# Kernel optimization log

Measured on AMD Instinct MI355X. Metric: run time of the kernel, lower is better.

The kernel has to match this reference:

```python
import jax, jax.numpy as jnp
import numpy as np

N_NODES = 20000
N_EDGES = 160000
N_GRAPHS = 16
NEG_INF = -1e30


def gcn_conv(x, edge_index, edge_weight, W, b):
    # PyG GCNConv with improved=True: add self-loops with weight 2.0,
    # symmetric degree normalization, linear transform, scatter-add aggregation.
    N = x.shape[0]
    row, col = edge_index[0], edge_index[1]
    loop = jnp.arange(N)
    row = jnp.concatenate([row, loop])
    col = jnp.concatenate([col, loop])
    ew = jnp.concatenate([edge_weight, jnp.full((N,), 2.0, edge_weight.dtype)])
    deg = jax.ops.segment_sum(ew, col, num_segments=N)
    dinv = jnp.where(deg > 0, deg ** -0.5, 0.0)  # deg_inv_sqrt, inf -> 0
    norm = dinv[row] * ew * dinv[col]            # [E+N]
    xl = x @ W                                   # [N, out]
    out = jax.ops.segment_sum(xl[row] * norm[:, None], col, num_segments=N)
    return out + b


def segment_softmax_masked(logits, mask, batch, num_segments):
    # softmax over masked entries, grouped by graph id (torch_geometric softmax
    # after masked_select); unmasked-out positions return 0.
    neg = jnp.asarray(NEG_INF, logits.dtype)
    ml = jnp.where(mask, logits, neg)
    mx = jax.ops.segment_max(ml, batch, num_segments=num_segments)
    ex = jnp.where(mask, jnp.exp(logits - mx[batch]), 0.0)
    s = jax.ops.segment_sum(ex, batch, num_segments=num_segments)
    return ex / jnp.maximum(s[batch], 1e-16)


def setup_inputs() -> dict:
    key = jax.random.key(0)
    ks = jax.random.split(key, 12)
    x = jax.random.normal(ks[0], (N_NODES, 5), dtype=jnp.float32)
    edge_index = jax.random.randint(ks[1], (2, N_EDGES), 0, N_NODES)
    edge_weight = jax.random.uniform(ks[2], (N_EDGES,), dtype=jnp.float32)
    mask = jax.random.randint(ks[3], (N_NODES,), 0, 2).astype(bool)
    batch = jnp.sort(jax.random.randint(ks[4], (N_NODES,), 0, N_GRAPHS))
    # parameters (Glorot-ish scaling)
    W1 = jax.random.normal(ks[5], (5, 1000), dtype=jnp.float32) / np.sqrt(5)
    b1 = jnp.zeros((1000,), jnp.float32)
    W2 = jax.random.normal(ks[6], (1000, 1000), dtype=jnp.float32) / np.sqrt(1000)
    b2 = jnp.zeros((1000,), jnp.float32)
    Wf = jax.random.normal(ks[7], (1000, 1), dtype=jnp.float32) / np.sqrt(1000)
    bf = jnp.zeros((1,), jnp.float32)
    return {"x": x, "edge_weight": edge_weight, "W1": W1, "b1": b1,
            "W2": W2, "b2": b2, "Wf": Wf, "bf": bf,
            "edge_index": edge_index, "mask": mask, "batch": batch}


def reference(x, edge_weight, W1, b1, W2, b2, Wf, bf, edge_index, mask, batch):
    h = jax.nn.relu(gcn_conv(x, edge_index, edge_weight, W1, b1))
    h = jax.nn.relu(gcn_conv(h, edge_index, edge_weight, W2, b2))
    # dropout treated as identity (eval mode) for a deterministic reference
    logits = (h @ Wf + bf)[:, 0]  # [N]
    return segment_softmax_masked(logits, mask, batch, N_GRAPHS)
```

## Files before the change

### kernel.cpp

```cpp
#include <hip/hip_runtime.h>

#define NN 20000
#define NE 160000
#define NG 16
#define KP 1024
#define MT2 160
#define MPAD2 (MT2*128)
#define NBLK 79

typedef __attribute__((ext_vector_type(8))) short bf16x8;
typedef __attribute__((ext_vector_type(4))) float f32x4;

#define GAS __attribute__((address_space(1)))
#define LAS __attribute__((address_space(3)))

__device__ __forceinline__ unsigned short f2bf(float f) {
    unsigned int u = __float_as_uint(f);
    u += 0x7FFFu + ((u >> 16) & 1u);
    return (unsigned short)(u >> 16);
}

__device__ __forceinline__ void gld_lds16(const char* g, char* l) {
    __builtin_amdgcn_global_load_lds((GAS void*)g, (LAS void*)l, 16, 0, 0);
}

__global__ void deg_cnt_kernel(const int* __restrict__ ei, const float* __restrict__ ew,
                               float* deg, int* cnt, const void* __restrict__ mask,
                               int* flags) {
    const int e = blockIdx.x * blockDim.x + threadIdx.x;
    if (e < 5000) {
        const unsigned v = ((const unsigned*)mask)[e];
        if (v > 1u) atomicOr(&flags[0], 1);
        if (v != 0u && v != 0x3F800000u) atomicOr(&flags[1], 1);
    }
    if (e >= NE) return;
    const int c = ei[NE + e];
    atomicAdd(&deg[c], ew[e]);
    atomicAdd(&cnt[c], 1);
}

__global__ __launch_bounds__(256) void partial_w2t_kernel(const int* __restrict__ cnt,
        const float* __restrict__ deg, const void* __restrict__ mask,
        const int* __restrict__ flags, int* __restrict__ mtmp,
        float* __restrict__ dinv, int* __restrict__ bcnt, int* __restrict__ bmsk,
        const float* __restrict__ W2, unsigned short* __restrict__ W2t,
        float* __restrict__ logitsC) {
    const int bid = blockIdx.x;
    const int t = threadIdx.x;
    if (bid < NBLK) {
        const int i = bid * 256 + t;
        const int f0 = flags[0], f1 = flags[1];
        int c = 0, mv = 0;
        if (i < NN) {
            c = cnt[i];
            dinv[i] = 1.0f / sqrtf(2.0f + deg[i]);
            if (f0 == 0)      mv = ((const int*)mask)[i] != 0;
            else if (f1 == 0) mv = ((const unsigned*)mask)[i] != 0u;
            else              mv = ((const unsigned char*)mask)[i] != 0;
            mtmp[i] = mv;
        }
        __shared__ int sc[256], sm[256];
        sc[t] = c; sm[t] = mv;
        __syncthreads();
        for (int off = 128; off; off >>= 1) {
            if (t < off) { sc[t] += sc[t + off]; sm[t] += sm[t + off]; }
            __syncthreads();
        }
        if (t == 0) { bcnt[bid] = sc[0]; bmsk[bid] = sm[0]; }
    } else {
        __shared__ float tile[32][33];
        const int bw = bid - NBLK;
        if (t < 20) logitsC[bw * 20 + t] = 0.0f;
        const int n0 = (bw & 31) * 32;
        const int k0 = (bw >> 5) * 32;
        const int tx = t & 31, ty = t >> 5;
#pragma unroll
        for (int j = 0; j < 4; ++j) {
            const int k = k0 + ty + j * 8;
            const int n = n0 + tx;
            tile[ty + j * 8][tx] = (k < 1000 && n < 1000) ? W2[k * 1000 + n] : 0.0f;
        }
        __syncthreads();
#pragma unroll
        for (int j = 0; j < 4; ++j) {
            const int n = n0 + ty + j * 8;
            const int k = k0 + tx;
            W2t[(size_t)n * KP + k] = f2bf(tile[tx][ty + j * 8]);
        }
    }
}

__global__ __launch_bounds__(256) void apply_kernel(const int* __restrict__ cnt,
        const int* __restrict__ mtmp, const int* __restrict__ bcnt,
        const int* __restrict__ bmsk, const int* __restrict__ batch,
        int* __restrict__ offs, int* __restrict__ perm, int* __restrict__ bc,
        int* __restrict__ nm, int* __restrict__ cursor, float* __restrict__ out) {
    const int b = blockIdx.x, t = threadIdx.x;
    __shared__ int pbc[128], pbm[128];
    if (t < 128) {
        pbc[t] = (t < NBLK) ? bcnt[t] : 0;
        pbm[t] = (t < NBLK) ? bmsk[t] : 0;
    }
    __syncthreads();
    for (int off = 1; off < 128; off <<= 1) {
        int uc = 0, um = 0;
        if (t < 128 && t >= off) { uc = pbc[t - off]; um = pbm[t - off]; }
        __syncthreads();
        if (t < 128) { pbc[t] += uc; pbm[t] += um; }
        __syncthreads();
    }
    if (b == 0 && t == 0) nm[0] = pbm[NBLK - 1];
    const int bco = (b == 0) ? 0 : pbc[b - 1];
    const int bmo = (b == 0) ? 0 : pbm[b - 1];
    const int i = b * 256 + t;
    const int c  = (i < NN) ? cnt[i]  : 0;
    const int mv = (i < NN) ? mtmp[i] : 0;
    __shared__ int sc[256], sm[256];
    sc[t] = c; sm[t] = mv;
    __syncthreads();
    for (int off = 1; off < 256; off <<= 1) {
        const int uc = (t >= off) ? sc[t - off] : 0;
        const int um = (t >= off) ? sm[t - off] : 0;
        __syncthreads();
        sc[t] += uc; sm[t] += um;
        __syncthreads();
    }
    if (i < NN) {
        cursor[i] = 0;
        out[i] = 0.0f;
        offs[i] = bco + sc[t] - c;
        if (mv) {
            const int pos = bmo + sm[t] - 1;
            perm[pos] = i;
            bc[pos] = batch[i];
        }
    }
}

__global__ void scatter_kernel(const int* __restrict__ ei, const float* __restrict__ ew,
                               const float* __restrict__ dinv, const int* __restrict__ offs,
                               int* cursor, int* __restrict__ ssrc, float* __restrict__ snorm) {
    const int e = blockIdx.x * blockDim.x + threadIdx.x;
    if (e >= NE) return;
    const int r = ei[e], c = ei[NE + e];
    const int pos = atomicAdd(&cursor[c], 1);
    const int idx = offs[c] + pos;
    ssrc[idx] = r;
    snorm[idx] = dinv[r] * ew[e] * dinv[c];
}

__global__ __launch_bounds__(256) void axf_kernel(const float* __restrict__ x,
        const int* __restrict__ ssrc, const float* __restrict__ snorm,
        const int* __restrict__ offs, const int* __restrict__ cnt,
        const float* __restrict__ dinv, float* __restrict__ Axf) {
    const int i = blockIdx.x * blockDim.x + threadIdx.x;
    if (i >= NN) return;
    float a0=0,a1=0,a2=0,a3=0,a4=0;
    const int s0 = offs[i], n = cnt[i];
    for (int e = s0; e < s0 + n; ++e) {
        const int r = ssrc[e];
        const float w = snorm[e];
        const float* xr = x + r * 5;
        a0 += w*xr[0]; a1 += w*xr[1]; a2 += w*xr[2]; a3 += w*xr[3]; a4 += w*xr[4];
    }
    const float wl = 2.0f * dinv[i] * dinv[i];
    const float* xi = x + i * 5;
    a0 += wl*xi[0]; a1 += wl*xi[1]; a2 += wl*xi[2]; a3 += wl*xi[3]; a4 += wl*xi[4];
    float* o = Axf + i * 5;
    o[0]=a0; o[1]=a1; o[2]=a2; o[3]=a3; o[4]=a4;
}

__global__ __launch_bounds__(256) void aggW1_kernel(const float* __restrict__ Axf,
        const float* __restrict__ W1, const float* __restrict__ b1,
        const int* __restrict__ ssrc, const float* __restrict__ snorm,
        const int* __restrict__ offs, const int* __restrict__ cnt,
        const float* __restrict__ dinv, const int* __restrict__ perm,
        const int* __restrict__ nm, unsigned short* __restrict__ G) {
    const int tid = threadIdx.x;
    const int wv = tid >> 6;
    const int lane = tid & 63;
    const int half = wv & 1;
    const int jbase = blockIdx.x * 8 + (wv >> 1) * 4;
    const int nmv = nm[0];
    const int npad = (nmv + 127) & ~127;
    if (jbase >= npad) return;

    const int c0 = half * 512 + lane * 8;
    float w1r[5][8], bbr[8];
#pragma unroll
    for (int q = 0; q < 2; ++q) {
        const int c = c0 + q * 4;
        const bool v = (c <= 996);
#pragma unroll
        for (int f = 0; f < 5; ++f) {
            const float4 w4 = v ? *(const float4*)(W1 + f * 1000 + c)
                                : make_float4(0.f, 0.f, 0.f, 0.f);
            w1r[f][q*4+0] = w4.x; w1r[f][q*4+1] = w4.y;
            w1r[f][q*4+2] = w4.z; w1r[f][q*4+3] = w4.w;
        }
        const float4 b4 = v ? *(const float4*)(b1 + c) : make_float4(0.f, 0.f, 0.f, 0.f);
        bbr[q*4+0] = b4.x; bbr[q*4+1] = b4.y; bbr[q*4+2] = b4.z; bbr[q*4+3] = b4.w;
    }

    int iv[4], s0a[4], na[4]; float dva[4];
#pragma unroll
    for (int d = 0; d < 4; ++d) {
        const int j = jbase + d;
        iv[d] = (j < nmv) ? perm[j] : -1;
    }
#pragma unroll
    for (int d = 0; d < 4; ++d) {
        if (iv[d] >= 0) { s0a[d] = offs[iv[d]]; na[d] = cnt[iv[d]]; dva[d] = dinv[iv[d]]; }
        else            { s0a[d] = 0; na[d] = -1; dva[d] = 0.f; }
    }

#pragma unroll
    for (int d = 0; d < 4; ++d) {
        const int j = jbase + d;
        float acc[8];
#pragma unroll
        for (int k = 0; k < 8; ++k) acc[k] = 0.f;
        const int i = iv[d];
        if (i >= 0) {
            const int s0 = s0a[d], n = na[d];
            const int total = n + 1;
            for (int base = 0; base < total; base += 64) {
                const int m = (total - base < 64) ? (total - base) : 64;
                float a0=0.f, a1=0.f, a2=0.f, a3=0.f, a4=0.f, we=0.f;
                if (lane < m) {
                    const int idx = base + lane;
                    int r;
                    if (idx < n) { r = ssrc[s0 + idx]; we = snorm[s0 + idx]; }
                    else         { r = i; we = 2.0f * dva[d] * dva[d]; }
                    const float* axr = Axf + r * 5;
                    a0 = axr[0]; a1 = axr[1]; a2 = axr[2]; a3 = axr[3]; a4 = axr[4];
                }
#pragma unroll 2
                for (int e = 0; e < m; ++e) {
                    const float s0v = __shfl(a0, e);
                    const float s1v = __shfl(a1, e);
                    const float s2v = __shfl(a2, e);
                    const float s3v = __shfl(a3, e);
                    const float s4v = __shfl(a4, e);
                    const float swv = __shfl(we, e);
#pragma unroll
                    for (int k = 0; k < 8; ++k) {
                        const float z = bbr[k] + s0v * w1r[0][k] + s1v * w1r[1][k]
                                      + s2v * w1r[2][k] + s3v * w1r[3][k] + s4v * w1r[4][k];
                        acc[k] += swv * fmaxf(z, 0.f);
                    }
                }
            }
        }
        bf16x8 pk;
#pragma unroll
        for (int k = 0; k < 8; ++k) pk[k] = (short)f2bf(acc[k]);
        *(bf16x8*)(G + (size_t)j * KP + c0) = pk;
    }
}

__global__ __launch_bounds__(256) void gemm_kernel(const unsigned short* __restrict__ A,
                                                   const unsigned short* __restrict__ B,
                                                   const float* __restrict__ b2,
                                                   const float* __restrict__ Wf,
                                                   const int* __restrict__ nm,
                                                   float* __restrict__ logitsC) {
    __shared__ unsigned short As[4096];
    __shared__ unsigned short Bs[4096];
    const int tid = threadIdx.x;
    __shared__ int s_nm;
    if (tid == 0) s_nm = nm[0];
    __syncthreads();
    const int nmv = s_nm;
    const int mstrips = (nmv + 127) >> 7;
    const int bid = blockIdx.x;
    const int tm = (bid >> 6) * 8 + (bid & 7);
    const int tn = (bid >> 3) & 7;
    if (tm >= mstrips) return;
    const int lane = tid & 63;
    const int wv = tid >> 6;
    const int wr = wv >> 1, wc = wv & 1;

    const int chunk = ((tid & 3) ^ ((tid >> 3) & 3)) * 16;
    const int rsub = tid >> 2;
    const char* Ag = (const char*)(A + (size_t)(tm * 128 + rsub) * KP) + chunk;
    const char* Bg = (const char*)(B + (size_t)(tn * 128 + rsub) * KP) + chunk;
    char* AsW = (char*)As + wv * 1024;
    char* BsW = (char*)Bs + wv * 1024;

    f32x4 acc[4][4];
#pragma unroll
    for (int i = 0; i < 4; ++i)
#pragma unroll
        for (int j = 0; j < 4; ++j) acc[i][j] = (f32x4){0.f, 0.f, 0.f, 0.f};

    const int m = lane & 15;
    const int quad = lane >> 4;
    const int sw = quad ^ ((m >> 1) & 3);
    const int aoff = (wr * 64 + m) * 64 + sw * 16;
    const int boff = (wc * 64 + m) * 64 + sw * 16;

    for (int kk = 0; kk < KP; kk += 32) {
        __syncthreads();
        const int kb = kk * 2;
        gld_lds16(Ag + kb,             AsW);
        gld_lds16(Ag + kb + 64 * 2048, AsW + 4096);
        gld_lds16(Bg + kb,             BsW);
        gld_lds16(Bg + kb + 64 * 2048, BsW + 4096);
        __syncthreads();
        bf16x8 af[4], bfv[4];
#pragma unroll
        for (int mt = 0; mt < 4; ++mt)
            af[mt] = *(const bf16x8*)((const char*)As + aoff + mt * 1024);
#pragma unroll
        for (int nt = 0; nt < 4; ++nt)
            bfv[nt] = *(const bf16x8*)((const char*)Bs + boff + nt * 1024);
#pragma unroll
        for (int mt = 0; mt < 4; ++mt)
#pragma unroll
            for (int nt = 0; nt < 4; ++nt)
                acc[mt][nt] = __builtin_amdgcn_mfma_f32_16x16x32_bf16(af[mt], bfv[nt], acc[mt][nt], 0, 0, 0);
    }

    const int col0 = tn * 128 + wc * 64 + m;
    const int row00 = tm * 128 + wr * 64 + quad * 4;
#pragma unroll
    for (int mt = 0; mt < 4; ++mt) {
        float ps0 = 0.f, ps1 = 0.f, ps2 = 0.f, ps3 = 0.f;
#pragma unroll
        for (int nt = 0; nt < 4; ++nt) {
            const int c = col0 + nt * 16;
            const float bbv = (c < 1000) ? b2[c] : 0.0f;
            const float wfv = (c < 1000) ? Wf[c] : 0.0f;
            ps0 += fmaxf(acc[mt][nt][0] + bbv, 0.f) * wfv;
            ps1 += fmaxf(acc[mt][nt][1] + bbv, 0.f) * wfv;
            ps2 += fmaxf(acc[mt][nt][2] + bbv, 0.f) * wfv;
            ps3 += fmaxf(acc[mt][nt][3] + bbv, 0.f) * wfv;
        }
#pragma unroll
        for (int msk = 1; msk < 16; msk <<= 1) {
            ps0 += __shfl_xor(ps0, msk);
            ps1 += __shfl_xor(ps1, msk);
            ps2 += __shfl_xor(ps2, msk);
            ps3 += __shfl_xor(ps3, msk);
        }
        if (m == 0) {
            const int row = row00 + mt * 16;
            if (row + 0 < nmv) atomicAdd(&logitsC[row + 0], ps0);
            if (row + 1 < nmv) atomicAdd(&logitsC[row + 1], ps1);
            if (row + 2 < nmv) atomicAdd(&logitsC[row + 2], ps2);
            if (row + 3 < nmv) atomicAdd(&logitsC[row + 3], ps3);
        }
    }
}

__global__ __launch_bounds__(256) void softmax_kernel(const float* __restrict__ logitsC,
        const int* __restrict__ perm, const int* __restrict__ bc,
        const int* __restrict__ nm, float* __restrict__ out) {
    const int g = blockIdx.x;
    const int t = threadIdx.x;
    __shared__ int s_lo, s_hi;
    __shared__ float red[4];
    __shared__ float sval;
    if (t == 0) {
        const int nmv = nm[0];
        int lo = 0, hi = nmv;
        while (lo < hi) { const int mid = (lo + hi) >> 1; if (bc[mid] < g) lo = mid + 1; else hi = mid; }
        s_lo = lo;
        int lo2 = lo, hi2 = nmv;
        while (lo2 < hi2) { const int mid = (lo2 + hi2) >> 1; if (bc[mid] < g + 1) lo2 = mid + 1; else hi2 = mid; }
        s_hi = lo2;
    }
    __syncthreads();
    const int lo = s_lo, hi = s_hi;
    float mx = -1e30f;
    for (int i = lo + t; i < hi; i += 256) mx = fmaxf(mx, logitsC[i]);
    for (int off = 32; off; off >>= 1) mx = fmaxf(mx, __shfl_down(mx, off));
    if ((t & 63) == 0) red[t >> 6] = mx;
    __syncthreads();
    if (t == 0) sval = fmaxf(fmaxf(red[0], red[1]), fmaxf(red[2], red[3]));
    __syncthreads();
    mx = sval;
    __syncthreads();
    float sm = 0.f;
    for (int i = lo + t; i < hi; i += 256) sm += expf(logitsC[i] - mx);
    for (int off = 32; off; off >>= 1) sm += __shfl_down(sm, off);
    if ((t & 63) == 0) red[t >> 6] = sm;
    __syncthreads();
    if (t == 0) sval = red[0] + red[1] + red[2] + red[3];
    __syncthreads();
    const float inv = 1.0f / fmaxf(sval, 1e-16f);
    for (int i = lo + t; i < hi; i += 256)
        out[perm[i]] = expf(logitsC[i] - mx) * inv;
}

extern "C" void kernel_launch(void* const* d_in, const int* in_sizes, int n_in,
                              void* d_out, int out_size, void* d_ws, size_t ws_size,
                              hipStream_t stream) {
    (void)in_sizes; (void)n_in; (void)out_size; (void)ws_size;
    const float* x   = (const float*)d_in[0];
    const float* ew  = (const float*)d_in[1];
    const float* W1  = (const float*)d_in[2];
    const float* b1  = (const float*)d_in[3];
    const float* W2  = (const float*)d_in[4];
    const float* b2  = (const float*)d_in[5];
    const float* Wf  = (const float*)d_in[6];
    const int*   ei  = (const int*)d_in[8];
    const void*  mask  = d_in[9];
    const int*   batch = (const int*)d_in[10];
    float* out = (float*)d_out;

    char* p = (char*)d_ws;
    auto carve = [&](size_t bytes) { char* q = p; p += (bytes + 255) & ~(size_t)255; return q; };
    char* zbase = p;
    float* deg     = (float*)carve(NN * 4);
    int*   cnt     = (int*)carve(NN * 4);
    int*   flags   = (int*)carve(256);
    size_t zspan = (size_t)(p - zbase);
    int*   cursor  = (int*)carve(NN * 4);
    float* logitsC = (float*)carve(MPAD2 * 4);
    int*   offs   = (int*)carve(NN * 4);
    float* dinv   = (float*)carve(NN * 4);
    int*   mtmp   = (int*)carve(NN * 4);
    int*   perm   = (int*)carve(NN * 4);
    int*   bc     = (int*)carve(NN * 4);
    int*   bcnt   = (int*)carve(NBLK * 4);
    int*   bmsk   = (int*)carve(NBLK * 4);
    int*   nmp    = (int*)carve(256);
    int*   ssrc   = (int*)carve(NE * 4);
    float* snorm  = (float*)carve(NE * 4);
    float* Axf    = (float*)carve(NN * 5 * 4);
    unsigned short* W2t = (unsigned short*)carve((size_t)KP * KP * 2);
    unsigned short* G   = (unsigned short*)carve((size_t)MPAD2 * KP * 2);

    hipMemsetAsync(zbase, 0, zspan, stream);
    hipLaunchKernelGGL(deg_cnt_kernel,     dim3(625),       dim3(256), 0, stream, ei, ew, deg, cnt, mask, flags);
    hipLaunchKernelGGL(partial_w2t_kernel, dim3(NBLK+1024), dim3(256), 0, stream, cnt, deg, mask, flags, mtmp, dinv, bcnt, bmsk, W2, W2t, logitsC);
    hipLaunchKernelGGL(apply_kernel,       dim3(NBLK),      dim3(256), 0, stream, cnt, mtmp, bcnt, bmsk, batch, offs, perm, bc, nmp, cursor, out);
    hipLaunchKernelGGL(scatter_kernel,     dim3(625),       dim3(256), 0, stream, ei, ew, dinv, offs, cursor, ssrc, snorm);
    hipLaunchKernelGGL(axf_kernel,         dim3(79),        dim3(256), 0, stream, x, ssrc, snorm, offs, cnt, dinv, Axf);
    hipLaunchKernelGGL(aggW1_kernel,       dim3(MPAD2/8),   dim3(256), 0, stream, Axf, W1, b1, ssrc, snorm, offs, cnt, dinv, perm, nmp, G);
    hipLaunchKernelGGL(gemm_kernel,        dim3(MT2*8),     dim3(256), 0, stream, G, W2t, b2, Wf, nmp, logitsC);
    hipLaunchKernelGGL(softmax_kernel,     dim3(NG),        dim3(256), 0, stream, logitsC, perm, bc, nmp, out);
}
```

Before: 198.5 us.

## Fuse preprocessing stages into one cooperative kernel with grid syncs

Merges the memset and five preprocessing kernels (degree count, partial sums plus W2 transpose, scan/apply, CSR scatter, first-layer aggregation) into a single cooperative kernel of 640 blocks, separated by grid-wide barriers. The W2 transpose now runs concurrently with the degree atomics on a disjoint set of blocks. The aim is to cut kernel launch and inter-kernel gaps. In exchange, each phase runs on a fixed grid with grid.sync costs, some phases use only 79 blocks, and cooperative launch has extra overhead.

```diff
diff --git a/kernel.cpp b/kernel.cpp
--- a/kernel.cpp
+++ b/kernel.cpp
@@ -1,4 +1,7 @@
 #include <hip/hip_runtime.h>
+#include <hip/hip_cooperative_groups.h>
+
+namespace cg = cooperative_groups;
 
 #define NN 20000
 #define NE 160000
@@ -7,6 +10,7 @@
 #define MT2 160
 #define MPAD2 (MT2*128)
 #define NBLK 79
+#define PREP_GRID 640
 
 typedef __attribute__((ext_vector_type(8))) short bf16x8;
 typedef __attribute__((ext_vector_type(4))) float f32x4;
@@ -24,31 +28,71 @@
     __builtin_amdgcn_global_load_lds((GAS void*)g, (LAS void*)l, 16, 0, 0);
 }
 
-__global__ void deg_cnt_kernel(const int* __restrict__ ei, const float* __restrict__ ew,
-                               float* deg, int* cnt, const void* __restrict__ mask,
-                               int* flags) {
-    const int e = blockIdx.x * blockDim.x + threadIdx.x;
-    if (e < 5000) {
-        const unsigned v = ((const unsigned*)mask)[e];
-        if (v > 1u) atomicOr(&flags[0], 1);
-        if (v != 0u && v != 0x3F800000u) atomicOr(&flags[1], 1);
-    }
-    if (e >= NE) return;
-    const int c = ei[NE + e];
-    atomicAdd(&deg[c], ew[e]);
-    atomicAdd(&cnt[c], 1);
-}
-
-__global__ __launch_bounds__(256) void partial_w2t_kernel(const int* __restrict__ cnt,
-        const float* __restrict__ deg, const void* __restrict__ mask,
-        const int* __restrict__ flags, int* __restrict__ mtmp,
-        float* __restrict__ dinv, int* __restrict__ bcnt, int* __restrict__ bmsk,
-        const float* __restrict__ W2, unsigned short* __restrict__ W2t,
+__global__ __launch_bounds__(256) void prep_kernel(
+        const int* __restrict__ ei, const float* __restrict__ ew,
+        const float* __restrict__ x, const float* __restrict__ W2,
+        const int* __restrict__ batch, const void* __restrict__ mask,
+        float* __restrict__ deg, int* __restrict__ cnt, int* __restrict__ flags,
+        int* __restrict__ mtmp, float* __restrict__ dinv,
+        int* __restrict__ bcnt, int* __restrict__ bmsk,
+        int* __restrict__ offs, int* __restrict__ perm, int* __restrict__ bc,
+        int* __restrict__ nm, int* __restrict__ cursor, float* __restrict__ out,
+        int* __restrict__ ssrc, float* __restrict__ snorm,
+        float* __restrict__ Axf, unsigned short* __restrict__ W2t,
         float* __restrict__ logitsC) {
+    cg::grid_group grid = cg::this_grid();
     const int bid = blockIdx.x;
     const int t = threadIdx.x;
-    if (bid < NBLK) {
-        const int i = bid * 256 + t;
+    const int nb = gridDim.x;
+    const int gt = bid * 256 + t;
+    const int gn = nb * 256;
+
+    __shared__ union ShU {
+        float tile[32][33];
+        struct { int sc[256]; int sm[256]; int pbc[128]; int pbm[128]; } s;
+    } sh;
+
+    for (int i = gt; i < NN; i += gn) { deg[i] = 0.0f; cnt[i] = 0; }
+    if (gt < 8) flags[gt] = 0;
+    grid.sync();
+
+    if (bid < 128) {
+        for (int vb = bid; vb < 1024; vb += 128) {
+            if (t < 20) logitsC[vb * 20 + t] = 0.0f;
+            const int n0 = (vb & 31) * 32;
+            const int k0 = (vb >> 5) * 32;
+            const int tx = t & 31, ty = t >> 5;
+            __syncthreads();
+#pragma unroll
+            for (int j = 0; j < 4; ++j) {
+                const int k = k0 + ty + j * 8;
+                const int n = n0 + tx;
+                sh.tile[ty + j * 8][tx] = (k < 1000 && n < 1000) ? W2[k * 1000 + n] : 0.0f;
+            }
+            __syncthreads();
+#pragma unroll
+            for (int j = 0; j < 4; ++j) {
+                const int n = n0 + ty + j * 8;
+                const int k = k0 + tx;
+                W2t[(size_t)n * KP + k] = f2bf(sh.tile[tx][ty + j * 8]);
+            }
+        }
+    } else {
+        for (int e = (bid - 128) * 256 + t; e < NE; e += (PREP_GRID - 128) * 256) {
+            if (e < 5000) {
+                const unsigned v = ((const unsigned*)mask)[e];
+                if (v > 1u) atomicOr(&flags[0], 1);
+                if (v != 0u && v != 0x3F800000u) atomicOr(&flags[1], 1);
+            }
+            const int c = ei[NE + e];
+            atomicAdd(&deg[c], ew[e]);
+            atomicAdd(&cnt[c], 1);
+        }
+    }
+    grid.sync();
+
+    for (int vb = bid; vb < NBLK; vb += nb) {
+        const int i = vb * 256 + t;
         const int f0 = flags[0], f1 = flags[1];
         int c = 0, mv = 0;
         if (i < NN) {
@@ -59,115 +103,83 @@
             else              mv = ((const unsigned char*)mask)[i] != 0;
             mtmp[i] = mv;
         }
-        __shared__ int sc[256], sm[256];
-        sc[t] = c; sm[t] = mv;
+        sh.s.sc[t] = c; sh.s.sm[t] = mv;
         __syncthreads();
         for (int off = 128; off; off >>= 1) {
-            if (t < off) { sc[t] += sc[t + off]; sm[t] += sm[t + off]; }
-            __syncthreads();
-        }
-        if (t == 0) { bcnt[bid] = sc[0]; bmsk[bid] = sm[0]; }
-    } else {
-        __shared__ float tile[32][33];
-        const int bw = bid - NBLK;
-        if (t < 20) logitsC[bw * 20 + t] = 0.0f;
-        const int n0 = (bw & 31) * 32;
-        const int k0 = (bw >> 5) * 32;
-        const int tx = t & 31, ty = t >> 5;
-#pragma unroll
-        for (int j = 0; j < 4; ++j) {
-            const int k = k0 + ty + j * 8;
-            const int n = n0 + tx;
-            tile[ty + j * 8][tx] = (k < 1000 && n < 1000) ? W2[k * 1000 + n] : 0.0f;
-        }
-        __syncthreads();
-#pragma unroll
-        for (int j = 0; j < 4; ++j) {
-            const int n = n0 + ty + j * 8;
-            const int k = k0 + tx;
-            W2t[(size_t)n * KP + k] = f2bf(tile[tx][ty + j * 8]);
-        }
-    }
-}
-
-__global__ __launch_bounds__(256) void apply_kernel(const int* __restrict__ cnt,
-        const int* __restrict__ mtmp, const int* __restrict__ bcnt,
-        const int* __restrict__ bmsk, const int* __restrict__ batch,
-        int* __restrict__ offs, int* __restrict__ perm, int* __restrict__ bc,
-        int* __restrict__ nm, int* __restrict__ cursor, float* __restrict__ out) {
-    const int b = blockIdx.x, t = threadIdx.x;
-    __shared__ int pbc[128], pbm[128];
-    if (t < 128) {
-        pbc[t] = (t < NBLK) ? bcnt[t] : 0;
-        pbm[t] = (t < NBLK) ? bmsk[t] : 0;
-    }
-    __syncthreads();
-    for (int off = 1; off < 128; off <<= 1) {
-        int uc = 0, um = 0;
-        if (t < 128 && t >= off) { uc = pbc[t - off]; um = pbm[t - off]; }
-        __syncthreads();
-        if (t < 128) { pbc[t] += uc; pbm[t] += um; }
-        __syncthreads();
-    }
-    if (b == 0 && t == 0) nm[0] = pbm[NBLK - 1];
-    const int bco = (b == 0) ? 0 : pbc[b - 1];
-    const int bmo = (b == 0) ? 0 : pbm[b - 1];
-    const int i = b * 256 + t;
-    const int c  = (i < NN) ? cnt[i]  : 0;
-    const int mv = (i < NN) ? mtmp[i] : 0;
-    __shared__ int sc[256], sm[256];
-    sc[t] = c; sm[t] = mv;
-    __syncthreads();
-    for (int off = 1; off < 256; off <<= 1) {
-        const int uc = (t >= off) ? sc[t - off] : 0;
-        const int um = (t >= off) ? sm[t - off] : 0;
-        __syncthreads();
-        sc[t] += uc; sm[t] += um;
-        __syncthreads();
-    }
-    if (i < NN) {
-        cursor[i] = 0;
-        out[i] = 0.0f;
-        offs[i] = bco + sc[t] - c;
-        if (mv) {
-            const int pos = bmo + sm[t] - 1;
-            perm[pos] = i;
-            bc[pos] = batch[i];
-        }
-    }
-}
-
-__global__ void scatter_kernel(const int* __restrict__ ei, const float* __restrict__ ew,
-                               const float* __restrict__ dinv, const int* __restrict__ offs,
-                               int* cursor, int* __restrict__ ssrc, float* __restrict__ snorm) {
-    const int e = blockIdx.x * blockDim.x + threadIdx.x;
-    if (e >= NE) return;
-    const int r = ei[e], c = ei[NE + e];
-    const int pos = atomicAdd(&cursor[c], 1);
-    const int idx = offs[c] + pos;
-    ssrc[idx] = r;
-    snorm[idx] = dinv[r] * ew[e] * dinv[c];
-}
-
-__global__ __launch_bounds__(256) void axf_kernel(const float* __restrict__ x,
-        const int* __restrict__ ssrc, const float* __restrict__ snorm,
-        const int* __restrict__ offs, const int* __restrict__ cnt,
-        const float* __restrict__ dinv, float* __restrict__ Axf) {
-    const int i = blockIdx.x * blockDim.x + threadIdx.x;
-    if (i >= NN) return;
-    float a0=0,a1=0,a2=0,a3=0,a4=0;
-    const int s0 = offs[i], n = cnt[i];
-    for (int e = s0; e < s0 + n; ++e) {
-        const int r = ssrc[e];
-        const float w = snorm[e];
-        const float* xr = x + r * 5;
-        a0 += w*xr[0]; a1 += w*xr[1]; a2 += w*xr[2]; a3 += w*xr[3]; a4 += w*xr[4];
-    }
-    const float wl = 2.0f * dinv[i] * dinv[i];
-    const float* xi = x + i * 5;
-    a0 += wl*xi[0]; a1 += wl*xi[1]; a2 += wl*xi[2]; a3 += wl*xi[3]; a4 += wl*xi[4];
-    float* o = Axf + i * 5;
-    o[0]=a0; o[1]=a1; o[2]=a2; o[3]=a3; o[4]=a4;
+            if (t < off) { sh.s.sc[t] += sh.s.sc[t + off]; sh.s.sm[t] += sh.s.sm[t + off]; }
+            __syncthreads();
+        }
+        if (t == 0) { bcnt[vb] = sh.s.sc[0]; bmsk[vb] = sh.s.sm[0]; }
+        __syncthreads();
+    }
+    grid.sync();
+
+    for (int vb = bid; vb < NBLK; vb += nb) {
+        if (t < 128) {
+            sh.s.pbc[t] = (t < NBLK) ? bcnt[t] : 0;
+            sh.s.pbm[t] = (t < NBLK) ? bmsk[t] : 0;
+        }
+        __syncthreads();
+        for (int off = 1; off < 128; off <<= 1) {
+            int uc = 0, um = 0;
+            if (t < 128 && t >= off) { uc = sh.s.pbc[t - off]; um = sh.s.pbm[t - off]; }
+            __syncthreads();
+            if (t < 128) { sh.s.pbc[t] += uc; sh.s.pbm[t] += um; }
+            __syncthreads();
+        }
+        if (vb == 0 && t == 0) nm[0] = sh.s.pbm[NBLK - 1];
+        const int bco = (vb == 0) ? 0 : sh.s.pbc[vb - 1];
+        const int bmo = (vb == 0) ? 0 : sh.s.pbm[vb - 1];
+        const int i = vb * 256 + t;
+        const int c  = (i < NN) ? cnt[i]  : 0;
+        const int mv = (i < NN) ? mtmp[i] : 0;
+        sh.s.sc[t] = c; sh.s.sm[t] = mv;
+        __syncthreads();
+        for (int off = 1; off < 256; off <<= 1) {
+            const int uc = (t >= off) ? sh.s.sc[t - off] : 0;
+            const int um = (t >= off) ? sh.s.sm[t - off] : 0;
+            __syncthreads();
+            sh.s.sc[t] += uc; sh.s.sm[t] += um;
+            __syncthreads();
+        }
+        if (i < NN) {
+            cursor[i] = 0;
+            out[i] = 0.0f;
+            offs[i] = bco + sh.s.sc[t] - c;
+            if (mv) {
+                const int pos = bmo + sh.s.sm[t] - 1;
+                perm[pos] = i;
+                bc[pos] = batch[i];
+            }
+        }
+        __syncthreads();
+    }
+    grid.sync();
+
+    for (int e = gt; e < NE; e += gn) {
+        const int r = ei[e], c = ei[NE + e];
+        const int pos = atomicAdd(&cursor[c], 1);
+        const int idx = offs[c] + pos;
+        ssrc[idx] = r;
+        snorm[idx] = dinv[r] * ew[e] * dinv[c];
+    }
+    grid.sync();
+
+    for (int i = gt; i < NN; i += gn) {
+        float a0 = 0, a1 = 0, a2 = 0, a3 = 0, a4 = 0;
+        const int s0 = offs[i], n = cnt[i];
+        for (int e = s0; e < s0 + n; ++e) {
+            const int r = ssrc[e];
+            const float w = snorm[e];
+            const float* xr = x + r * 5;
+            a0 += w * xr[0]; a1 += w * xr[1]; a2 += w * xr[2]; a3 += w * xr[3]; a4 += w * xr[4];
+        }
+        const float wl = 2.0f * dinv[i] * dinv[i];
+        const float* xi = x + i * 5;
+        a0 += wl * xi[0]; a1 += wl * xi[1]; a2 += wl * xi[2]; a3 += wl * xi[3]; a4 += wl * xi[4];
+        float* o = Axf + i * 5;
+        o[0] = a0; o[1] = a1; o[2] = a2; o[3] = a3; o[4] = a4;
+    }
 }
 
 __global__ __launch_bounds__(256) void aggW1_kernel(const float* __restrict__ Axf,
@@ -412,11 +424,9 @@
 
     char* p = (char*)d_ws;
     auto carve = [&](size_t bytes) { char* q = p; p += (bytes + 255) & ~(size_t)255; return q; };
-    char* zbase = p;
     float* deg     = (float*)carve(NN * 4);
     int*   cnt     = (int*)carve(NN * 4);
     int*   flags   = (int*)carve(256);
-    size_t zspan = (size_t)(p - zbase);
     int*   cursor  = (int*)carve(NN * 4);
     float* logitsC = (float*)carve(MPAD2 * 4);
     int*   offs   = (int*)carve(NN * 4);
@@ -433,13 +443,19 @@
     unsigned short* W2t = (unsigned short*)carve((size_t)KP * KP * 2);
     unsigned short* G   = (unsigned short*)carve((size_t)MPAD2 * KP * 2);
 
-    hipMemsetAsync(zbase, 0, zspan, stream);
-    hipLaunchKernelGGL(deg_cnt_kernel,     dim3(625),       dim3(256), 0, stream, ei, ew, deg, cnt, mask, flags);
-    hipLaunchKernelGGL(partial_w2t_kernel, dim3(NBLK+1024), dim3(256), 0, stream, cnt, deg, mask, flags, mtmp, dinv, bcnt, bmsk, W2, W2t, logitsC);
-    hipLaunchKernelGGL(apply_kernel,       dim3(NBLK),      dim3(256), 0, stream, cnt, mtmp, bcnt, bmsk, batch, offs, perm, bc, nmp, cursor, out);
-    hipLaunchKernelGGL(scatter_kernel,     dim3(625),       dim3(256), 0, stream, ei, ew, dinv, offs, cursor, ssrc, snorm);
-    hipLaunchKernelGGL(axf_kernel,         dim3(79),        dim3(256), 0, stream, x, ssrc, snorm, offs, cnt, dinv, Axf);
-    hipLaunchKernelGGL(aggW1_kernel,       dim3(MPAD2/8),   dim3(256), 0, stream, Axf, W1, b1, ssrc, snorm, offs, cnt, dinv, perm, nmp, G);
-    hipLaunchKernelGGL(gemm_kernel,        dim3(MT2*8),     dim3(256), 0, stream, G, W2t, b2, Wf, nmp, logitsC);
-    hipLaunchKernelGGL(softmax_kernel,     dim3(NG),        dim3(256), 0, stream, logitsC, perm, bc, nmp, out);
-}
+    void* pargs[] = {
+        (void*)&ei, (void*)&ew, (void*)&x, (void*)&W2, (void*)&batch, (void*)&mask,
+        (void*)&deg, (void*)&cnt, (void*)&flags, (void*)&mtmp, (void*)&dinv,
+        (void*)&bcnt, (void*)&bmsk, (void*)&offs, (void*)&perm, (void*)&bc,
+        (void*)&nmp, (void*)&cursor, (void*)&out, (void*)&ssrc, (void*)&snorm,
+        (void*)&Axf, (void*)&W2t, (void*)&logitsC
+    };
+    hipLaunchCooperativeKernel((void*)prep_kernel, dim3(PREP_GRID), dim3(256),
+                               pargs, 0, stream);
+    hipLaunchKernelGGL(aggW1_kernel, dim3(MPAD2/8), dim3(256), 0, stream,
+                       Axf, W1, b1, ssrc, snorm, offs, cnt, dinv, perm, nmp, G);
+    hipLaunchKernelGGL(gemm_kernel,  dim3(MT2*8),   dim3(256), 0, stream,
+                       G, W2t, b2, Wf, nmp, logitsC);
+    hipLaunchKernelGGL(softmax_kernel, dim3(NG),    dim3(256), 0, stream,
+                       logitsC, perm, bc, nmp, out);
+}
```

After: 560.7 us. 2.82x slower.

## Merge scan into single-block mid kernel and fuse Axf into edge scatter

Applied to the files above, without the earlier changes.

Replaces the two-kernel block-partial/apply prefix scan with a single-block serial-per-thread scan inside a combined kernel that also computes dinv, zeroes Axf and transposes W2. The Axf aggregation is folded into the edge scatter kernel using float atomics, removing the separate axf pass. This cuts launch count and kernel boundaries but introduces a one-block scan with strided, uncoalesced reads on the critical path and many float atomics with nondeterministic summation order.

```diff
diff --git a/kernel.cpp b/kernel.cpp
--- a/kernel.cpp
+++ b/kernel.cpp
@@ -39,40 +39,70 @@
     atomicAdd(&cnt[c], 1);
 }
 
-__global__ __launch_bounds__(256) void partial_w2t_kernel(const int* __restrict__ cnt,
-        const float* __restrict__ deg, const void* __restrict__ mask,
-        const int* __restrict__ flags, int* __restrict__ mtmp,
-        float* __restrict__ dinv, int* __restrict__ bcnt, int* __restrict__ bmsk,
-        const float* __restrict__ W2, unsigned short* __restrict__ W2t,
-        float* __restrict__ logitsC) {
+__global__ __launch_bounds__(256) void mid_kernel(
+        const float* __restrict__ deg, const int* __restrict__ cnt,
+        const int* __restrict__ flags, const void* __restrict__ mask,
+        const int* __restrict__ batch, const float* __restrict__ W2,
+        float* __restrict__ dinv, float* __restrict__ Axf,
+        int* __restrict__ offs, int* __restrict__ perm, int* __restrict__ bcv,
+        int* __restrict__ nm, int* __restrict__ cursor, float* __restrict__ out,
+        unsigned short* __restrict__ W2t, float* __restrict__ logitsC) {
     const int bid = blockIdx.x;
     const int t = threadIdx.x;
-    if (bid < NBLK) {
-        const int i = bid * 256 + t;
+    __shared__ float tile[32][33];
+    __shared__ int wtc[4], wtm[4];
+
+    if (bid == 0) {
         const int f0 = flags[0], f1 = flags[1];
-        int c = 0, mv = 0;
+        const bool wordmask = (f0 == 0 || f1 == 0);
+        const int lane = t & 63, wvi = t >> 6;
+        const int i0 = t * 79;
+        int tc = 0, tm = 0;
+        for (int j = 0; j < 79; ++j) {
+            const int i = i0 + j;
+            if (i < NN) {
+                tc += cnt[i];
+                tm += wordmask ? (((const unsigned*)mask)[i] != 0u)
+                               : (((const unsigned char*)mask)[i] != 0);
+            }
+        }
+        const int myc = tc, mym = tm;
+        for (int o = 1; o < 64; o <<= 1) {
+            const int uc = __shfl_up(tc, o);
+            const int um = __shfl_up(tm, o);
+            if (lane >= o) { tc += uc; tm += um; }
+        }
+        if (lane == 63) { wtc[wvi] = tc; wtm[wvi] = tm; }
+        __syncthreads();
+        int bc0 = 0, bm0 = 0;
+        for (int w = 0; w < wvi; ++w) { bc0 += wtc[w]; bm0 += wtm[w]; }
+        int runc = bc0 + tc - myc;
+        int runm = bm0 + tm - mym;
+        if (t == 0) nm[0] = wtm[0] + wtm[1] + wtm[2] + wtm[3];
+        for (int j = 0; j < 79; ++j) {
+            const int i = i0 + j;
+            if (i < NN) {
+                const int c = cnt[i];
+                const int mv = wordmask ? (((const unsigned*)mask)[i] != 0u)
+                                        : (((const unsigned char*)mask)[i] != 0);
+                offs[i] = runc; runc += c;
+                cursor[i] = 0;
+                out[i] = 0.0f;
+                if (mv) { perm[runm] = i; bcv[runm] = batch[i]; ++runm; }
+            }
+        }
+    } else if (bid < 80) {
+        const int i = (bid - 1) * 256 + t;
         if (i < NN) {
-            c = cnt[i];
             dinv[i] = 1.0f / sqrtf(2.0f + deg[i]);
-            if (f0 == 0)      mv = ((const int*)mask)[i] != 0;
-            else if (f1 == 0) mv = ((const unsigned*)mask)[i] != 0u;
-            else              mv = ((const unsigned char*)mask)[i] != 0;
-            mtmp[i] = mv;
-        }
-        __shared__ int sc[256], sm[256];
-        sc[t] = c; sm[t] = mv;
-        __syncthreads();
-        for (int off = 128; off; off >>= 1) {
-            if (t < off) { sc[t] += sc[t + off]; sm[t] += sm[t + off]; }
-            __syncthreads();
-        }
-        if (t == 0) { bcnt[bid] = sc[0]; bmsk[bid] = sm[0]; }
+            float* a = Axf + i * 5;
+            a[0] = 0.f; a[1] = 0.f; a[2] = 0.f; a[3] = 0.f; a[4] = 0.f;
+        }
     } else {
-        __shared__ float tile[32][33];
-        const int bw = bid - NBLK;
-        if (t < 20) logitsC[bw * 20 + t] = 0.0f;
-        const int n0 = (bw & 31) * 32;
-        const int k0 = (bw >> 5) * 32;
+        const int vb = bid - 80;
+        if (t < 20) logitsC[vb * 20 + t] = 0.0f;
+        const int n0 = (vb & 31) * 32;
+        const int k0 = (vb >> 5) * 32;
         const int tx = t & 31, ty = t >> 5;
 #pragma unroll
         for (int j = 0; j < 4; ++j) {
@@ -90,84 +120,37 @@
     }
 }
 
-__global__ __launch_bounds__(256) void apply_kernel(const int* __restrict__ cnt,
-        const int* __restrict__ mtmp, const int* __restrict__ bcnt,
-        const int* __restrict__ bmsk, const int* __restrict__ batch,
-        int* __restrict__ offs, int* __restrict__ perm, int* __restrict__ bc,
-        int* __restrict__ nm, int* __restrict__ cursor, float* __restrict__ out) {
-    const int b = blockIdx.x, t = threadIdx.x;
-    __shared__ int pbc[128], pbm[128];
-    if (t < 128) {
-        pbc[t] = (t < NBLK) ? bcnt[t] : 0;
-        pbm[t] = (t < NBLK) ? bmsk[t] : 0;
-    }
-    __syncthreads();
-    for (int off = 1; off < 128; off <<= 1) {
-        int uc = 0, um = 0;
-        if (t < 128 && t >= off) { uc = pbc[t - off]; um = pbm[t - off]; }
-        __syncthreads();
-        if (t < 128) { pbc[t] += uc; pbm[t] += um; }
-        __syncthreads();
-    }
-    if (b == 0 && t == 0) nm[0] = pbm[NBLK - 1];
-    const int bco = (b == 0) ? 0 : pbc[b - 1];
-    const int bmo = (b == 0) ? 0 : pbm[b - 1];
-    const int i = b * 256 + t;
-    const int c  = (i < NN) ? cnt[i]  : 0;
-    const int mv = (i < NN) ? mtmp[i] : 0;
-    __shared__ int sc[256], sm[256];
-    sc[t] = c; sm[t] = mv;
-    __syncthreads();
-    for (int off = 1; off < 256; off <<= 1) {
-        const int uc = (t >= off) ? sc[t - off] : 0;
-        const int um = (t >= off) ? sm[t - off] : 0;
-        __syncthreads();
-        sc[t] += uc; sm[t] += um;
-        __syncthreads();
-    }
-    if (i < NN) {
-        cursor[i] = 0;
-        out[i] = 0.0f;
-        offs[i] = bco + sc[t] - c;
-        if (mv) {
-            const int pos = bmo + sm[t] - 1;
-            perm[pos] = i;
-            bc[pos] = batch[i];
-        }
-    }
-}
-
-__global__ void scatter_kernel(const int* __restrict__ ei, const float* __restrict__ ew,
-                               const float* __restrict__ dinv, const int* __restrict__ offs,
-                               int* cursor, int* __restrict__ ssrc, float* __restrict__ snorm) {
+__global__ void scatter_axf_kernel(const int* __restrict__ ei, const float* __restrict__ ew,
+                                   const float* __restrict__ x, const float* __restrict__ dinv,
+                                   const int* __restrict__ offs, int* cursor,
+                                   int* __restrict__ ssrc, float* __restrict__ snorm,
+                                   float* __restrict__ Axf) {
     const int e = blockIdx.x * blockDim.x + threadIdx.x;
-    if (e >= NE) return;
-    const int r = ei[e], c = ei[NE + e];
-    const int pos = atomicAdd(&cursor[c], 1);
-    const int idx = offs[c] + pos;
-    ssrc[idx] = r;
-    snorm[idx] = dinv[r] * ew[e] * dinv[c];
-}
-
-__global__ __launch_bounds__(256) void axf_kernel(const float* __restrict__ x,
-        const int* __restrict__ ssrc, const float* __restrict__ snorm,
-        const int* __restrict__ offs, const int* __restrict__ cnt,
-        const float* __restrict__ dinv, float* __restrict__ Axf) {
-    const int i = blockIdx.x * blockDim.x + threadIdx.x;
-    if (i >= NN) return;
-    float a0=0,a1=0,a2=0,a3=0,a4=0;
-    const int s0 = offs[i], n = cnt[i];
-    for (int e = s0; e < s0 + n; ++e) {
-        const int r = ssrc[e];
-        const float w = snorm[e];
+    if (e < NE) {
+        const int r = ei[e], c = ei[NE + e];
+        const int pos = atomicAdd(&cursor[c], 1);
+        const int idx = offs[c] + pos;
+        const float w = dinv[r] * ew[e] * dinv[c];
+        ssrc[idx] = r;
+        snorm[idx] = w;
         const float* xr = x + r * 5;
-        a0 += w*xr[0]; a1 += w*xr[1]; a2 += w*xr[2]; a3 += w*xr[3]; a4 += w*xr[4];
-    }
-    const float wl = 2.0f * dinv[i] * dinv[i];
-    const float* xi = x + i * 5;
-    a0 += wl*xi[0]; a1 += wl*xi[1]; a2 += wl*xi[2]; a3 += wl*xi[3]; a4 += wl*xi[4];
-    float* o = Axf + i * 5;
-    o[0]=a0; o[1]=a1; o[2]=a2; o[3]=a3; o[4]=a4;
+        float* ac = Axf + c * 5;
+        atomicAdd(ac + 0, w * xr[0]);
+        atomicAdd(ac + 1, w * xr[1]);
+        atomicAdd(ac + 2, w * xr[2]);
+        atomicAdd(ac + 3, w * xr[3]);
+        atomicAdd(ac + 4, w * xr[4]);
+    }
+    if (e < NN) {
+        const float wl = 2.0f * dinv[e] * dinv[e];
+        const float* xi = x + e * 5;
+        float* ai = Axf + e * 5;
+        atomicAdd(ai + 0, wl * xi[0]);
+        atomicAdd(ai + 1, wl * xi[1]);
+        atomicAdd(ai + 2, wl * xi[2]);
+        atomicAdd(ai + 3, wl * xi[3]);
+        atomicAdd(ai + 4, wl * xi[4]);
+    }
 }
 
 __global__ __launch_bounds__(256) void aggW1_kernel(const float* __restrict__ Axf,
@@ -421,11 +404,8 @@
     float* logitsC = (float*)carve(MPAD2 * 4);
     int*   offs   = (int*)carve(NN * 4);
     float* dinv   = (float*)carve(NN * 4);
-    int*   mtmp   = (int*)carve(NN * 4);
     int*   perm   = (int*)carve(NN * 4);
     int*   bc     = (int*)carve(NN * 4);
-    int*   bcnt   = (int*)carve(NBLK * 4);
-    int*   bmsk   = (int*)carve(NBLK * 4);
     int*   nmp    = (int*)carve(256);
     int*   ssrc   = (int*)carve(NE * 4);
     float* snorm  = (float*)carve(NE * 4);
@@ -434,12 +414,10 @@
     unsigned short* G   = (unsigned short*)carve((size_t)MPAD2 * KP * 2);
 
     hipMemsetAsync(zbase, 0, zspan, stream);
-    hipLaunchKernelGGL(deg_cnt_kernel,     dim3(625),       dim3(256), 0, stream, ei, ew, deg, cnt, mask, flags);
-    hipLaunchKernelGGL(partial_w2t_kernel, dim3(NBLK+1024), dim3(256), 0, stream, cnt, deg, mask, flags, mtmp, dinv, bcnt, bmsk, W2, W2t, logitsC);
-    hipLaunchKernelGGL(apply_kernel,       dim3(NBLK),      dim3(256), 0, stream, cnt, mtmp, bcnt, bmsk, batch, offs, perm, bc, nmp, cursor, out);
-    hipLaunchKernelGGL(scatter_kernel,     dim3(625),       dim3(256), 0, stream, ei, ew, dinv, offs, cursor, ssrc, snorm);
-    hipLaunchKernelGGL(axf_kernel,         dim3(79),        dim3(256), 0, stream, x, ssrc, snorm, offs, cnt, dinv, Axf);
-    hipLaunchKernelGGL(aggW1_kernel,       dim3(MPAD2/8),   dim3(256), 0, stream, Axf, W1, b1, ssrc, snorm, offs, cnt, dinv, perm, nmp, G);
-    hipLaunchKernelGGL(gemm_kernel,        dim3(MT2*8),     dim3(256), 0, stream, G, W2t, b2, Wf, nmp, logitsC);
-    hipLaunchKernelGGL(softmax_kernel,     dim3(NG),        dim3(256), 0, stream, logitsC, perm, bc, nmp, out);
-}
+    hipLaunchKernelGGL(deg_cnt_kernel,   dim3(625),     dim3(256), 0, stream, ei, ew, deg, cnt, mask, flags);
+    hipLaunchKernelGGL(mid_kernel,       dim3(1104),    dim3(256), 0, stream, deg, cnt, flags, mask, batch, W2, dinv, Axf, offs, perm, bc, nmp, cursor, out, W2t, logitsC);
+    hipLaunchKernelGGL(scatter_axf_kernel, dim3(625),   dim3(256), 0, stream, ei, ew, x, dinv, offs, cursor, ssrc, snorm, Axf);
+    hipLaunchKernelGGL(aggW1_kernel,     dim3(MPAD2/8), dim3(256), 0, stream, Axf, W1, b1, ssrc, snorm, offs, cnt, dinv, perm, nmp, G);
+    hipLaunchKernelGGL(gemm_kernel,      dim3(MT2*8),   dim3(256), 0, stream, G, W2t, b2, Wf, nmp, logitsC);
+    hipLaunchKernelGGL(softmax_kernel,   dim3(NG),      dim3(256), 0, stream, logitsC, perm, bc, nmp, out);
+}
```

Result: slower. 350.6 us (+76.6%).

## Merge degree counting with W2 transpose, redo prefix scan, double GEMM K-step

Applied to the files above, without the earlier changes.

The edge degree/count atomics now run in the same launch as the W2 bf16 transpose, so those independent jobs share one grid. The block-partial reduction kernel is dropped: each apply block re-reduces all preceding counts and mask values itself, and a small kernel computes dinv. The GEMM loads a K-slice of 64 per iteration into doubled LDS tiles, halving the barrier count. The trade-off is redundant prefix work in the apply kernel (up to about 20K reads for the last blocks), more LDS per GEMM block that may lower occupancy, and the same number of launches overall.

```diff
diff --git a/kernel.cpp b/kernel.cpp
--- a/kernel.cpp
+++ b/kernel.cpp
@@ -24,55 +24,30 @@
     __builtin_amdgcn_global_load_lds((GAS void*)g, (LAS void*)l, 16, 0, 0);
 }
 
-__global__ void deg_cnt_kernel(const int* __restrict__ ei, const float* __restrict__ ew,
-                               float* deg, int* cnt, const void* __restrict__ mask,
-                               int* flags) {
-    const int e = blockIdx.x * blockDim.x + threadIdx.x;
-    if (e < 5000) {
-        const unsigned v = ((const unsigned*)mask)[e];
-        if (v > 1u) atomicOr(&flags[0], 1);
-        if (v != 0u && v != 0x3F800000u) atomicOr(&flags[1], 1);
-    }
-    if (e >= NE) return;
-    const int c = ei[NE + e];
-    atomicAdd(&deg[c], ew[e]);
-    atomicAdd(&cnt[c], 1);
-}
-
-__global__ __launch_bounds__(256) void partial_w2t_kernel(const int* __restrict__ cnt,
-        const float* __restrict__ deg, const void* __restrict__ mask,
-        const int* __restrict__ flags, int* __restrict__ mtmp,
-        float* __restrict__ dinv, int* __restrict__ bcnt, int* __restrict__ bmsk,
+__global__ __launch_bounds__(256) void degcnt_w2t_kernel(
+        const int* __restrict__ ei, const float* __restrict__ ew,
+        const void* __restrict__ mask, float* deg, int* cnt, int* flags,
         const float* __restrict__ W2, unsigned short* __restrict__ W2t,
         float* __restrict__ logitsC) {
     const int bid = blockIdx.x;
     const int t = threadIdx.x;
-    if (bid < NBLK) {
-        const int i = bid * 256 + t;
-        const int f0 = flags[0], f1 = flags[1];
-        int c = 0, mv = 0;
-        if (i < NN) {
-            c = cnt[i];
-            dinv[i] = 1.0f / sqrtf(2.0f + deg[i]);
-            if (f0 == 0)      mv = ((const int*)mask)[i] != 0;
-            else if (f1 == 0) mv = ((const unsigned*)mask)[i] != 0u;
-            else              mv = ((const unsigned char*)mask)[i] != 0;
-            mtmp[i] = mv;
-        }
-        __shared__ int sc[256], sm[256];
-        sc[t] = c; sm[t] = mv;
-        __syncthreads();
-        for (int off = 128; off; off >>= 1) {
-            if (t < off) { sc[t] += sc[t + off]; sm[t] += sm[t + off]; }
-            __syncthreads();
-        }
-        if (t == 0) { bcnt[bid] = sc[0]; bmsk[bid] = sm[0]; }
+    __shared__ float tile[32][33];
+    if (bid < 625) {
+        const int e = bid * 256 + t;
+        if (e < 5000) {
+            const unsigned v = ((const unsigned*)mask)[e];
+            if (v > 1u) atomicOr(&flags[0], 1);
+            if (v != 0u && v != 0x3F800000u) atomicOr(&flags[1], 1);
+        }
+        if (e >= NE) return;
+        const int c = ei[NE + e];
+        atomicAdd(&deg[c], ew[e]);
+        atomicAdd(&cnt[c], 1);
     } else {
-        __shared__ float tile[32][33];
-        const int bw = bid - NBLK;
-        if (t < 20) logitsC[bw * 20 + t] = 0.0f;
-        const int n0 = (bw & 31) * 32;
-        const int k0 = (bw >> 5) * 32;
+        const int vb = bid - 625;
+        if (t < 20) logitsC[vb * 20 + t] = 0.0f;
+        const int n0 = (vb & 31) * 32;
+        const int k0 = (vb >> 5) * 32;
         const int tx = t & 31, ty = t >> 5;
 #pragma unroll
         for (int j = 0; j < 4; ++j) {
@@ -91,31 +66,36 @@
 }
 
 __global__ __launch_bounds__(256) void apply_kernel(const int* __restrict__ cnt,
-        const int* __restrict__ mtmp, const int* __restrict__ bcnt,
-        const int* __restrict__ bmsk, const int* __restrict__ batch,
-        int* __restrict__ offs, int* __restrict__ perm, int* __restrict__ bc,
-        int* __restrict__ nm, int* __restrict__ cursor, float* __restrict__ out) {
+        const void* __restrict__ mask, const int* __restrict__ flags,
+        const int* __restrict__ batch, int* __restrict__ offs,
+        int* __restrict__ perm, int* __restrict__ bc, int* __restrict__ nm,
+        int* __restrict__ cursor, float* __restrict__ out) {
     const int b = blockIdx.x, t = threadIdx.x;
-    __shared__ int pbc[128], pbm[128];
-    if (t < 128) {
-        pbc[t] = (t < NBLK) ? bcnt[t] : 0;
-        pbm[t] = (t < NBLK) ? bmsk[t] : 0;
-    }
-    __syncthreads();
-    for (int off = 1; off < 128; off <<= 1) {
-        int uc = 0, um = 0;
-        if (t < 128 && t >= off) { uc = pbc[t - off]; um = pbm[t - off]; }
-        __syncthreads();
-        if (t < 128) { pbc[t] += uc; pbm[t] += um; }
-        __syncthreads();
-    }
-    if (b == 0 && t == 0) nm[0] = pbm[NBLK - 1];
-    const int bco = (b == 0) ? 0 : pbc[b - 1];
-    const int bmo = (b == 0) ? 0 : pbm[b - 1];
+    const int f0 = flags[0], f1 = flags[1];
+    const bool wordmask = (f0 == 0 || f1 == 0);
+    const int lim = b * 256;
+    int pc = 0, pm = 0;
+    for (int i = t; i < lim; i += 256) {
+        pc += cnt[i];
+        pm += wordmask ? (((const unsigned*)mask)[i] != 0u)
+                       : (((const unsigned char*)mask)[i] != 0);
+    }
+    __shared__ int sc[256], sm[256];
+    sc[t] = pc; sm[t] = pm;
+    __syncthreads();
+    for (int off = 128; off; off >>= 1) {
+        if (t < off) { sc[t] += sc[t + off]; sm[t] += sm[t + off]; }
+        __syncthreads();
+    }
+    const int bco = sc[0], bmo = sm[0];
+    __syncthreads();
     const int i = b * 256 + t;
-    const int c  = (i < NN) ? cnt[i]  : 0;
-    const int mv = (i < NN) ? mtmp[i] : 0;
-    __shared__ int sc[256], sm[256];
+    int c = 0, mv = 0;
+    if (i < NN) {
+        c = cnt[i];
+        mv = wordmask ? (((const unsigned*)mask)[i] != 0u)
+                      : (((const unsigned char*)mask)[i] != 0);
+    }
     sc[t] = c; sm[t] = mv;
     __syncthreads();
     for (int off = 1; off < 256; off <<= 1) {
@@ -135,6 +115,7 @@
             bc[pos] = batch[i];
         }
     }
+    if (b == NBLK - 1 && t == 255) nm[0] = bmo + sm[255];
 }
 
 __global__ void scatter_kernel(const int* __restrict__ ei, const float* __restrict__ ew,
@@ -147,6 +128,12 @@
     const int idx = offs[c] + pos;
     ssrc[idx] = r;
     snorm[idx] = dinv[r] * ew[e] * dinv[c];
+}
+
+__global__ __launch_bounds__(256) void dinv_kernel(const float* __restrict__ deg,
+                                                   float* __restrict__ dinv) {
+    const int i = blockIdx.x * blockDim.x + threadIdx.x;
+    if (i < NN) dinv[i] = 1.0f / sqrtf(2.0f + deg[i]);
 }
 
 __global__ __launch_bounds__(256) void axf_kernel(const float* __restrict__ x,
@@ -265,8 +252,8 @@
                                                    const float* __restrict__ Wf,
                                                    const int* __restrict__ nm,
                                                    float* __restrict__ logitsC) {
-    __shared__ unsigned short As[4096];
-    __shared__ unsigned short Bs[4096];
+    __shared__ unsigned short As[8192];
+    __shared__ unsigned short Bs[8192];
     const int tid = threadIdx.x;
     __shared__ int s_nm;
     if (tid == 0) s_nm = nm[0];
@@ -300,26 +287,34 @@
     const int aoff = (wr * 64 + m) * 64 + sw * 16;
     const int boff = (wc * 64 + m) * 64 + sw * 16;
 
-    for (int kk = 0; kk < KP; kk += 32) {
+    for (int kk = 0; kk < KP; kk += 64) {
         __syncthreads();
         const int kb = kk * 2;
-        gld_lds16(Ag + kb,             AsW);
-        gld_lds16(Ag + kb + 64 * 2048, AsW + 4096);
-        gld_lds16(Bg + kb,             BsW);
-        gld_lds16(Bg + kb + 64 * 2048, BsW + 4096);
-        __syncthreads();
-        bf16x8 af[4], bfv[4];
-#pragma unroll
-        for (int mt = 0; mt < 4; ++mt)
-            af[mt] = *(const bf16x8*)((const char*)As + aoff + mt * 1024);
-#pragma unroll
-        for (int nt = 0; nt < 4; ++nt)
-            bfv[nt] = *(const bf16x8*)((const char*)Bs + boff + nt * 1024);
-#pragma unroll
-        for (int mt = 0; mt < 4; ++mt)
+        gld_lds16(Ag + kb,                  AsW);
+        gld_lds16(Ag + kb + 64 * 2048,      AsW + 4096);
+        gld_lds16(Ag + kb + 64,             AsW + 8192);
+        gld_lds16(Ag + kb + 64 + 64 * 2048, AsW + 8192 + 4096);
+        gld_lds16(Bg + kb,                  BsW);
+        gld_lds16(Bg + kb + 64 * 2048,      BsW + 4096);
+        gld_lds16(Bg + kb + 64,             BsW + 8192);
+        gld_lds16(Bg + kb + 64 + 64 * 2048, BsW + 8192 + 4096);
+        __syncthreads();
+#pragma unroll
+        for (int h = 0; h < 2; ++h) {
+            const int hb = h * 8192;
+            bf16x8 af[4], bfv[4];
+#pragma unroll
+            for (int mt = 0; mt < 4; ++mt)
+                af[mt] = *(const bf16x8*)((const char*)As + hb + aoff + mt * 1024);
 #pragma unroll
             for (int nt = 0; nt < 4; ++nt)
-                acc[mt][nt] = __builtin_amdgcn_mfma_f32_16x16x32_bf16(af[mt], bfv[nt], acc[mt][nt], 0, 0, 0);
+                bfv[nt] = *(const bf16x8*)((const char*)Bs + hb + boff + nt * 1024);
+#pragma unroll
+            for (int mt = 0; mt < 4; ++mt)
+#pragma unroll
+                for (int nt = 0; nt < 4; ++nt)
+                    acc[mt][nt] = __builtin_amdgcn_mfma_f32_16x16x32_bf16(af[mt], bfv[nt], acc[mt][nt], 0, 0, 0);
+        }
     }
 
     const int col0 = tn * 128 + wc * 64 + m;
@@ -421,11 +416,8 @@
     float* logitsC = (float*)carve(MPAD2 * 4);
     int*   offs   = (int*)carve(NN * 4);
     float* dinv   = (float*)carve(NN * 4);
-    int*   mtmp   = (int*)carve(NN * 4);
     int*   perm   = (int*)carve(NN * 4);
     int*   bc     = (int*)carve(NN * 4);
-    int*   bcnt   = (int*)carve(NBLK * 4);
-    int*   bmsk   = (int*)carve(NBLK * 4);
     int*   nmp    = (int*)carve(256);
     int*   ssrc   = (int*)carve(NE * 4);
     float* snorm  = (float*)carve(NE * 4);
@@ -434,12 +426,12 @@
     unsigned short* G   = (unsigned short*)carve((size_t)MPAD2 * KP * 2);
 
     hipMemsetAsync(zbase, 0, zspan, stream);
-    hipLaunchKernelGGL(deg_cnt_kernel,     dim3(625),       dim3(256), 0, stream, ei, ew, deg, cnt, mask, flags);
-    hipLaunchKernelGGL(partial_w2t_kernel, dim3(NBLK+1024), dim3(256), 0, stream, cnt, deg, mask, flags, mtmp, dinv, bcnt, bmsk, W2, W2t, logitsC);
-    hipLaunchKernelGGL(apply_kernel,       dim3(NBLK),      dim3(256), 0, stream, cnt, mtmp, bcnt, bmsk, batch, offs, perm, bc, nmp, cursor, out);
-    hipLaunchKernelGGL(scatter_kernel,     dim3(625),       dim3(256), 0, stream, ei, ew, dinv, offs, cursor, ssrc, snorm);
-    hipLaunchKernelGGL(axf_kernel,         dim3(79),        dim3(256), 0, stream, x, ssrc, snorm, offs, cnt, dinv, Axf);
-    hipLaunchKernelGGL(aggW1_kernel,       dim3(MPAD2/8),   dim3(256), 0, stream, Axf, W1, b1, ssrc, snorm, offs, cnt, dinv, perm, nmp, G);
-    hipLaunchKernelGGL(gemm_kernel,        dim3(MT2*8),     dim3(256), 0, stream, G, W2t, b2, Wf, nmp, logitsC);
-    hipLaunchKernelGGL(softmax_kernel,     dim3(NG),        dim3(256), 0, stream, logitsC, perm, bc, nmp, out);
-}
+    hipLaunchKernelGGL(degcnt_w2t_kernel, dim3(1649),   dim3(256), 0, stream, ei, ew, mask, deg, cnt, flags, W2, W2t, logitsC);
+    hipLaunchKernelGGL(dinv_kernel,       dim3(NBLK),   dim3(256), 0, stream, deg, dinv);
+    hipLaunchKernelGGL(apply_kernel,      dim3(NBLK),   dim3(256), 0, stream, cnt, mask, flags, batch, offs, perm, bc, nmp, cursor, out);
+    hipLaunchKernelGGL(scatter_kernel,    dim3(625),    dim3(256), 0, stream, ei, ew, dinv, offs, cursor, ssrc, snorm);
+    hipLaunchKernelGGL(axf_kernel,        dim3(NBLK),   dim3(256), 0, stream, x, ssrc, snorm, offs, cnt, dinv, Axf);
+    hipLaunchKernelGGL(aggW1_kernel,      dim3(MPAD2/8),dim3(256), 0, stream, Axf, W1, b1, ssrc, snorm, offs, cnt, dinv, perm, nmp, G);
+    hipLaunchKernelGGL(gemm_kernel,       dim3(MT2*8),  dim3(256), 0, stream, G, W2t, b2, Wf, nmp, logitsC);
+    hipLaunchKernelGGL(softmax_kernel,    dim3(NG),     dim3(256), 0, stream, logitsC, perm, bc, nmp, out);
+}
```

After: 232.1 us. 16.9% more time.
